# Optimization experiments

Measured on AMD Instinct MI355X. Metric: run time of the kernel, lower is better.

Reference implementation:

```python
import jax, jax.numpy as jnp
import numpy as np

IN_SIZE, HIDDEN, OUT_SIZE, BATCH = 4096, 4096, 1024, 8192


def setup_inputs() -> dict:
    key = jax.random.key(0)
    ks = jax.random.split(key, 7)
    def lin_init(kw, kb, fan_in, fan_out):
        bound = 1.0 / np.sqrt(fan_in)
        w = jax.random.uniform(kw, (fan_out, fan_in), jnp.float32, -bound, bound)
        b = jax.random.uniform(kb, (fan_out,), jnp.float32, -bound, bound)
        return w, b
    w1, b1 = lin_init(ks[0], ks[1], IN_SIZE, HIDDEN)
    w2, b2 = lin_init(ks[2], ks[3], HIDDEN, HIDDEN)
    w3, b3 = lin_init(ks[4], ks[5], HIDDEN, OUT_SIZE)
    x = jax.random.normal(ks[6], (BATCH, IN_SIZE), jnp.float32)
    return {"x": x, "w1": w1, "b1": b1, "w2": w2, "b2": b2, "w3": w3, "b3": b3}


def binarize(w):
    # sign(w) * mean(|w|), scalar scale over the whole tensor
    return jnp.sign(w) * jnp.mean(jnp.abs(w))


def reference(x, w1, b1, w2, b2, w3, b3):
    h = jax.nn.relu(x @ binarize(w1).T + b1)
    h = jax.nn.relu(h @ binarize(w2).T + b2)
    return jax.nn.sigmoid(h @ binarize(w3).T + b3)
```

## Files before the change

### kernel.cpp

```cpp
#include <hip/hip_runtime.h>


typedef __bf16 bf16x8 __attribute__((ext_vector_type(8)));
typedef float  f32x4  __attribute__((ext_vector_type(4)));
typedef unsigned short ushort_t;

#define AS1 __attribute__((address_space(1)))
#define AS3 __attribute__((address_space(3)))

__device__ __forceinline__ void async16(const void* g, AS3 void* l) {
    __builtin_amdgcn_global_load_lds((AS1 void*)const_cast<void*>(g), l, 16, 0, 0);
}

__device__ __forceinline__ ushort_t f2bf(float f) {
    unsigned u = __float_as_uint(f);
    u += 0x7FFFu + ((u >> 16) & 1u);
    return (ushort_t)(u >> 16);
}

__global__ void zero3_kernel(float* p) {
    if (threadIdx.x < 3) p[threadIdx.x] = 0.f;
}

__global__ __launch_bounds__(256) void absmean_kernel(const float4* __restrict__ w,
                                                      int n4, float* __restrict__ out) {
    float s = 0.f;
    for (int i = blockIdx.x * blockDim.x + threadIdx.x; i < n4; i += gridDim.x * blockDim.x) {
        float4 v = w[i];
        s += fabsf(v.x) + fabsf(v.y) + fabsf(v.z) + fabsf(v.w);
    }
#pragma unroll
    for (int off = 32; off > 0; off >>= 1) s += __shfl_down(s, off);
    __shared__ float wsum[4];
    if ((threadIdx.x & 63) == 0) wsum[threadIdx.x >> 6] = s;
    __syncthreads();
    if (threadIdx.x == 0) atomicAdd(out, wsum[0] + wsum[1] + wsum[2] + wsum[3]);
}

__global__ __launch_bounds__(256) void sign_kernel(const float4* __restrict__ w,
                                                   ushort4* __restrict__ s, int n4) {
    for (int i = blockIdx.x * blockDim.x + threadIdx.x; i < n4; i += gridDim.x * blockDim.x) {
        float4 v = w[i];
        ushort4 o;
        o.x = v.x > 0.f ? 0x3F80u : (v.x < 0.f ? 0xBF80u : 0u);
        o.y = v.y > 0.f ? 0x3F80u : (v.y < 0.f ? 0xBF80u : 0u);
        o.z = v.z > 0.f ? 0x3F80u : (v.z < 0.f ? 0xBF80u : 0u);
        o.w = v.w > 0.f ? 0x3F80u : (v.w < 0.f ? 0xBF80u : 0u);
        s[i] = o;
    }
}

__global__ __launch_bounds__(256) void cvt_kernel(const float4* __restrict__ x,
                                                  ushort4* __restrict__ o, int n4) {
    for (int i = blockIdx.x * blockDim.x + threadIdx.x; i < n4; i += gridDim.x * blockDim.x) {
        float4 v = x[i];
        ushort4 u;
        u.x = f2bf(v.x); u.y = f2bf(v.y); u.z = f2bf(v.z); u.w = f2bf(v.w);
        o[i] = u;
    }
}

template <int ACT>
__global__ __launch_bounds__(256) void gemm_bwn(const ushort_t* __restrict__ A,
                                                const ushort_t* __restrict__ B,
                                                const float* __restrict__ sumptr, float inv_n,
                                                const float* __restrict__ bias,
                                                void* __restrict__ out,
                                                int M, int N, int K) {
    __shared__ __align__(16) ushort_t As[128 * 32];
    __shared__ __align__(16) ushort_t Bs[128 * 32];

    const int t    = threadIdx.x;
    const int lane = t & 63;
    const int w    = t >> 6;
    const int tm   = blockIdx.y, tn = blockIdx.x;

    const int   srow  = t >> 2;
    const int   scolb = (t & 3) * 16;
    const char* Abase = (const char*)A + ((size_t)(tm * 128 + srow) * K) * 2 + scolb;
    const char* Bbase = (const char*)B + ((size_t)(tn * 128 + srow) * K) * 2 + scolb;
    const size_t rowskip = (size_t)64 * K * 2;

    AS3 char* lA = (AS3 char*)As;
    AS3 char* lB = (AS3 char*)Bs;
    const int lbase = w * 1024;

    const int fr = lane & 15;
    const int fk = (lane >> 4) * 16;
    const int rm = (w >> 1) * 64;
    const int rn = (w & 1) * 64;

    f32x4 acc[4][4] = {};

    for (int kt = 0; kt < K; kt += 32) {
        __syncthreads();
        const size_t ko = (size_t)kt * 2;
        async16(Abase + ko,           lA + lbase);
        async16(Abase + rowskip + ko, lA + lbase + 4096);
        async16(Bbase + ko,           lB + lbase);
        async16(Bbase + rowskip + ko, lB + lbase + 4096);
        __syncthreads();

        bf16x8 af[4], bf[4];
#pragma unroll
        for (int i = 0; i < 4; ++i)
            af[i] = *(const bf16x8*)((const char*)As + (rm + i * 16 + fr) * 64 + fk);
#pragma unroll
        for (int j = 0; j < 4; ++j)
            bf[j] = *(const bf16x8*)((const char*)Bs + (rn + j * 16 + fr) * 64 + fk);
#pragma unroll
        for (int i = 0; i < 4; ++i)
#pragma unroll
            for (int j = 0; j < 4; ++j)
                acc[i][j] = __builtin_amdgcn_mfma_f32_16x16x32_bf16(af[i], bf[j], acc[i][j], 0, 0, 0);
    }

    const float scale = sumptr[0] * inv_n;
    const int   r0    = (lane >> 4) * 4;
#pragma unroll
    for (int j = 0; j < 4; ++j) {
        const int   col = tn * 128 + rn + j * 16 + fr;
        const float bj  = bias[col];
#pragma unroll
        for (int i = 0; i < 4; ++i) {
            const int rowb = tm * 128 + rm + i * 16 + r0;
#pragma unroll
            for (int r = 0; r < 4; ++r) {
                float v = acc[i][j][r] * scale + bj;
                if (ACT == 0) {
                    v = fmaxf(v, 0.f);
                    ((ushort_t*)out)[(size_t)(rowb + r) * N + col] = f2bf(v);
                } else {
                    v = 1.f / (1.f + __expf(-v));
                    ((float*)out)[(size_t)(rowb + r) * N + col] = v;
                }
            }
        }
    }
}

extern "C" void kernel_launch(void* const* d_in, const int* in_sizes, int n_in,
                              void* d_out, int out_size, void* d_ws, size_t ws_size,
                              hipStream_t stream) {
    const float* x  = (const float*)d_in[0];
    const float* w1 = (const float*)d_in[1];
    const float* b1 = (const float*)d_in[2];
    const float* w2 = (const float*)d_in[3];
    const float* b2 = (const float*)d_in[4];
    const float* w3 = (const float*)d_in[5];
    const float* b3 = (const float*)d_in[6];

    const size_t MB = 1024ull * 1024ull;
    char* ws = (char*)d_ws;
    float*    scales = (float*)ws;
    ushort_t* bufA = (ushort_t*)(ws + 256);
    ushort_t* bufB = (ushort_t*)(ws + 256 + 64 * MB);
    ushort_t* bufC = (ushort_t*)(ws + 256 + 128 * MB);

    zero3_kernel<<<1, 64, 0, stream>>>(scales);

    absmean_kernel<<<2048, 256, 0, stream>>>((const float4*)w1, 16777216 / 4, scales + 0);
    absmean_kernel<<<2048, 256, 0, stream>>>((const float4*)w2, 16777216 / 4, scales + 1);
    absmean_kernel<<<1024, 256, 0, stream>>>((const float4*)w3, 4194304 / 4, scales + 2);

    sign_kernel<<<2048, 256, 0, stream>>>((const float4*)w1, (ushort4*)bufC, 16777216 / 4);
    cvt_kernel<<<2048, 256, 0, stream>>>((const float4*)x, (ushort4*)bufA, 33554432 / 4);
    gemm_bwn<0><<<dim3(32, 64), 256, 0, stream>>>(bufA, bufC, scales + 0, 1.f / 16777216.f,
                                                  b1, bufB, 8192, 4096, 4096);

    sign_kernel<<<2048, 256, 0, stream>>>((const float4*)w2, (ushort4*)bufC, 16777216 / 4);
    gemm_bwn<0><<<dim3(32, 64), 256, 0, stream>>>(bufB, bufC, scales + 1, 1.f / 16777216.f,
                                                  b2, bufA, 8192, 4096, 4096);

    sign_kernel<<<1024, 256, 0, stream>>>((const float4*)w3, (ushort4*)bufC, 4194304 / 4);
    gemm_bwn<1><<<dim3(8, 64), 256, 0, stream>>>(bufA, bufC, scales + 2, 1.f / 4194304.f,
                                                 b3, d_out, 8192, 1024, 4096);
}
```

Before: 1.144 ms.

## Add pipelined 256x256 double-buffered GEMM and fuse absmean with sign conversion

Adds a new 512-thread GEMM kernel with 256x256 output tiles and a 64-wide K step. It double-buffers A and B in 128KB of swizzled LDS, interleaves async global-to-LDS loads with four MFMA quadrants, and raises wave priority during the MFMA phases. This kernel replaces the 128x128 single-buffer GEMM for the two large layers, aiming to raise data reuse and hide load latency. Separately, the abs-mean reduction is fused into the sign conversion kernel so each weight tensor is read once instead of twice. The risk is lower occupancy from the large LDS use and the fragility of the hand-written waitcnt and barrier scheduling.

New measurement: 934.4 us. 1.22x faster.

```diff
diff --git a/kernel.cpp b/kernel.cpp
--- a/kernel.cpp
+++ b/kernel.cpp
@@ -22,25 +22,13 @@
     if (threadIdx.x < 3) p[threadIdx.x] = 0.f;
 }
 
-__global__ __launch_bounds__(256) void absmean_kernel(const float4* __restrict__ w,
-                                                      int n4, float* __restrict__ out) {
-    float s = 0.f;
+__global__ __launch_bounds__(256) void binarize_kernel(const float4* __restrict__ w,
+                                                       ushort4* __restrict__ s, int n4,
+                                                       float* __restrict__ out) {
+    float acc = 0.f;
     for (int i = blockIdx.x * blockDim.x + threadIdx.x; i < n4; i += gridDim.x * blockDim.x) {
         float4 v = w[i];
-        s += fabsf(v.x) + fabsf(v.y) + fabsf(v.z) + fabsf(v.w);
-    }
-#pragma unroll
-    for (int off = 32; off > 0; off >>= 1) s += __shfl_down(s, off);
-    __shared__ float wsum[4];
-    if ((threadIdx.x & 63) == 0) wsum[threadIdx.x >> 6] = s;
-    __syncthreads();
-    if (threadIdx.x == 0) atomicAdd(out, wsum[0] + wsum[1] + wsum[2] + wsum[3]);
-}
-
-__global__ __launch_bounds__(256) void sign_kernel(const float4* __restrict__ w,
-                                                   ushort4* __restrict__ s, int n4) {
-    for (int i = blockIdx.x * blockDim.x + threadIdx.x; i < n4; i += gridDim.x * blockDim.x) {
-        float4 v = w[i];
+        acc += fabsf(v.x) + fabsf(v.y) + fabsf(v.z) + fabsf(v.w);
         ushort4 o;
         o.x = v.x > 0.f ? 0x3F80u : (v.x < 0.f ? 0xBF80u : 0u);
         o.y = v.y > 0.f ? 0x3F80u : (v.y < 0.f ? 0xBF80u : 0u);
@@ -48,6 +36,12 @@
         o.w = v.w > 0.f ? 0x3F80u : (v.w < 0.f ? 0xBF80u : 0u);
         s[i] = o;
     }
+#pragma unroll
+    for (int off = 32; off > 0; off >>= 1) acc += __shfl_down(acc, off);
+    __shared__ float wsum[4];
+    if ((threadIdx.x & 63) == 0) wsum[threadIdx.x >> 6] = acc;
+    __syncthreads();
+    if (threadIdx.x == 0) atomicAdd(out, wsum[0] + wsum[1] + wsum[2] + wsum[3]);
 }
 
 __global__ __launch_bounds__(256) void cvt_kernel(const float4* __restrict__ x,
@@ -57,6 +51,170 @@
         ushort4 u;
         u.x = f2bf(v.x); u.y = f2bf(v.y); u.z = f2bf(v.z); u.w = f2bf(v.w);
         o[i] = u;
+    }
+}
+
+template <int ACT>
+__global__ __launch_bounds__(512, 2) void gemm256(const ushort_t* __restrict__ A,
+                                                  const ushort_t* __restrict__ B,
+                                                  const float* __restrict__ sumptr, float inv_n,
+                                                  const float* __restrict__ bias,
+                                                  void* __restrict__ out,
+                                                  int M, int N, int K) {
+    __shared__ __align__(16) char smem[131072];
+
+    const int T    = threadIdx.x;
+    const int lane = T & 63;
+    const int w    = T >> 6;
+    const int wm   = w >> 2, wn = w & 3;
+    const int bm   = blockIdx.y * 256;
+    const int bn   = blockIdx.x * 256;
+
+    const size_t ldab = (size_t)K * 2;
+
+    const int srow = T >> 3;
+    const int cswz = ((T & 7) << 4) ^ ((srow & 7) << 4);
+    const char*  Ag = (const char*)A + (size_t)(bm + srow) * ldab + cswz;
+    const char*  Bg = (const char*)B + (size_t)(bn + srow) * ldab + cswz;
+    const size_t half_rows = 128 * ldab, l1_rows = 64 * ldab;
+
+    AS3 char* lds  = (AS3 char*)smem;
+    const int dstw = w * 1024;
+
+    auto stageA = [&](int s, int h) {
+        const char* src = Ag + (size_t)h * half_rows + (size_t)s * 128;
+        AS3 char*   d   = lds + (s & 1) * 65536 + h * 16384 + dstw;
+        async16(src, d);
+        async16(src + l1_rows, d + 8192);
+    };
+    auto stageB = [&](int s, int h) {
+        const char* src = Bg + (size_t)h * half_rows + (size_t)s * 128;
+        AS3 char*   d   = lds + (s & 1) * 65536 + 32768 + h * 16384 + dstw;
+        async16(src, d);
+        async16(src + l1_rows, d + 8192);
+    };
+
+    const int axor = (lane & 7) << 4;
+    const int arow = wm * 128 + (lane & 15);
+    const int brow = wn * 64 + (lane & 15);
+    const int kb   = (lane >> 4) * 16;
+
+    f32x4 acc[8][4] = {};
+    const int NT = K >> 6;
+
+    stageB(0, 0); stageB(0, 1); stageA(0, 0); stageA(0, 1);
+    stageB(1, 0); stageB(1, 1);
+    asm volatile("s_waitcnt vmcnt(4)" ::: "memory");
+    __builtin_amdgcn_s_barrier();
+
+    for (int t = 0; t < NT; ++t) {
+        const char* As_ = (const char*)smem + (t & 1) * 65536;
+        const char* Bs_ = As_ + 32768;
+
+        bf16x8 a0[4][2], a1[4][2], b0[2][2], b1[2][2];
+
+#pragma unroll
+        for (int m = 0; m < 4; ++m)
+#pragma unroll
+            for (int kk = 0; kk < 2; ++kk)
+                a0[m][kk] = *(const bf16x8*)(As_ + (arow + m * 16) * 128 + ((kk * 64 + kb) ^ axor));
+#pragma unroll
+        for (int n = 0; n < 2; ++n)
+#pragma unroll
+            for (int kk = 0; kk < 2; ++kk)
+                b0[n][kk] = *(const bf16x8*)(Bs_ + (brow + n * 16) * 128 + ((kk * 64 + kb) ^ axor));
+        if (t + 1 < NT) stageA(t + 1, 0);
+        __builtin_amdgcn_s_barrier();
+        asm volatile("s_waitcnt lgkmcnt(0)");
+        __builtin_amdgcn_s_setprio(1);
+#pragma unroll
+        for (int m = 0; m < 4; ++m)
+#pragma unroll
+            for (int n = 0; n < 2; ++n)
+#pragma unroll
+                for (int kk = 0; kk < 2; ++kk)
+                    acc[m][n] = __builtin_amdgcn_mfma_f32_16x16x32_bf16(a0[m][kk], b0[n][kk], acc[m][n], 0, 0, 0);
+        __builtin_amdgcn_s_setprio(0);
+        __builtin_amdgcn_s_barrier();
+
+#pragma unroll
+        for (int n = 0; n < 2; ++n)
+#pragma unroll
+            for (int kk = 0; kk < 2; ++kk)
+                b1[n][kk] = *(const bf16x8*)(Bs_ + (brow + 32 + n * 16) * 128 + ((kk * 64 + kb) ^ axor));
+        if (t + 1 < NT) stageA(t + 1, 1);
+        __builtin_amdgcn_s_barrier();
+        asm volatile("s_waitcnt lgkmcnt(0)");
+        __builtin_amdgcn_s_setprio(1);
+#pragma unroll
+        for (int m = 0; m < 4; ++m)
+#pragma unroll
+            for (int n = 0; n < 2; ++n)
+#pragma unroll
+                for (int kk = 0; kk < 2; ++kk)
+                    acc[m][n + 2] = __builtin_amdgcn_mfma_f32_16x16x32_bf16(a0[m][kk], b1[n][kk], acc[m][n + 2], 0, 0, 0);
+        __builtin_amdgcn_s_setprio(0);
+        __builtin_amdgcn_s_barrier();
+
+#pragma unroll
+        for (int m = 0; m < 4; ++m)
+#pragma unroll
+            for (int kk = 0; kk < 2; ++kk)
+                a1[m][kk] = *(const bf16x8*)(As_ + (arow + 64 + m * 16) * 128 + ((kk * 64 + kb) ^ axor));
+        if (t + 2 < NT) stageB(t + 2, 0);
+        __builtin_amdgcn_s_barrier();
+        asm volatile("s_waitcnt lgkmcnt(0)");
+        __builtin_amdgcn_s_setprio(1);
+#pragma unroll
+        for (int m = 0; m < 4; ++m)
+#pragma unroll
+            for (int n = 0; n < 2; ++n)
+#pragma unroll
+                for (int kk = 0; kk < 2; ++kk)
+                    acc[m + 4][n] = __builtin_amdgcn_mfma_f32_16x16x32_bf16(a1[m][kk], b0[n][kk], acc[m + 4][n], 0, 0, 0);
+        __builtin_amdgcn_s_setprio(0);
+        __builtin_amdgcn_s_barrier();
+
+        if (t + 2 < NT) stageB(t + 2, 1);
+        __builtin_amdgcn_s_barrier();
+        __builtin_amdgcn_s_setprio(1);
+#pragma unroll
+        for (int m = 0; m < 4; ++m)
+#pragma unroll
+            for (int n = 0; n < 2; ++n)
+#pragma unroll
+                for (int kk = 0; kk < 2; ++kk)
+                    acc[m + 4][n + 2] = __builtin_amdgcn_mfma_f32_16x16x32_bf16(a1[m][kk], b1[n][kk], acc[m + 4][n + 2], 0, 0, 0);
+        __builtin_amdgcn_s_setprio(0);
+        if (t < NT - 2) {
+            asm volatile("s_waitcnt vmcnt(4)" ::: "memory");
+        } else {
+            asm volatile("s_waitcnt vmcnt(0)" ::: "memory");
+        }
+        __builtin_amdgcn_s_barrier();
+    }
+
+    const float scale = sumptr[0] * inv_n;
+    const int   r0    = (lane >> 4) * 4;
+#pragma unroll
+    for (int nj = 0; nj < 4; ++nj) {
+        const int   col = bn + wn * 64 + nj * 16 + (lane & 15);
+        const float bj  = bias[col];
+#pragma unroll
+        for (int mi = 0; mi < 8; ++mi) {
+            const int rowb = bm + wm * 128 + mi * 16 + r0;
+#pragma unroll
+            for (int r = 0; r < 4; ++r) {
+                float v = acc[mi][nj][r] * scale + bj;
+                if (ACT == 0) {
+                    v = fmaxf(v, 0.f);
+                    ((ushort_t*)out)[(size_t)(rowb + r) * N + col] = f2bf(v);
+                } else {
+                    v = 1.f / (1.f + __expf(-v));
+                    ((float*)out)[(size_t)(rowb + r) * N + col] = v;
+                }
+            }
+        }
     }
 }
 
@@ -159,20 +317,19 @@
 
     zero3_kernel<<<1, 64, 0, stream>>>(scales);
 
-    absmean_kernel<<<2048, 256, 0, stream>>>((const float4*)w1, 16777216 / 4, scales + 0);
-    absmean_kernel<<<2048, 256, 0, stream>>>((const float4*)w2, 16777216 / 4, scales + 1);
-    absmean_kernel<<<1024, 256, 0, stream>>>((const float4*)w3, 4194304 / 4, scales + 2);
-
-    sign_kernel<<<2048, 256, 0, stream>>>((const float4*)w1, (ushort4*)bufC, 16777216 / 4);
+    binarize_kernel<<<2048, 256, 0, stream>>>((const float4*)w1, (ushort4*)bufC,
+                                              16777216 / 4, scales + 0);
     cvt_kernel<<<2048, 256, 0, stream>>>((const float4*)x, (ushort4*)bufA, 33554432 / 4);
-    gemm_bwn<0><<<dim3(32, 64), 256, 0, stream>>>(bufA, bufC, scales + 0, 1.f / 16777216.f,
-                                                  b1, bufB, 8192, 4096, 4096);
-
-    sign_kernel<<<2048, 256, 0, stream>>>((const float4*)w2, (ushort4*)bufC, 16777216 / 4);
-    gemm_bwn<0><<<dim3(32, 64), 256, 0, stream>>>(bufB, bufC, scales + 1, 1.f / 16777216.f,
-                                                  b2, bufA, 8192, 4096, 4096);
-
-    sign_kernel<<<1024, 256, 0, stream>>>((const float4*)w3, (ushort4*)bufC, 4194304 / 4);
+    gemm256<0><<<dim3(16, 32), 512, 0, stream>>>(bufA, bufC, scales + 0, 1.f / 16777216.f,
+                                                 b1, bufB, 8192, 4096, 4096);
+
+    binarize_kernel<<<2048, 256, 0, stream>>>((const float4*)w2, (ushort4*)bufC,
+                                              16777216 / 4, scales + 1);
+    gemm256<0><<<dim3(16, 32), 512, 0, stream>>>(bufB, bufC, scales + 1, 1.f / 16777216.f,
+                                                 b2, bufA, 8192, 4096, 4096);
+
+    binarize_kernel<<<1024, 256, 0, stream>>>((const float4*)w3, (ushort4*)bufC,
+                                              4194304 / 4, scales + 2);
     gemm_bwn<1><<<dim3(8, 64), 256, 0, stream>>>(bufA, bufC, scales + 2, 1.f / 4194304.f,
                                                  b3, d_out, 8192, 1024, 4096);
 }
```
